# Performance work log

Hardware: AMD Instinct MI355X
Metric: run time of the kernel (lower is better)

Reference implementation:

```python
import jax, jax.numpy as jnp
import numpy as np

DIM = 768
NUM_HEADS = 12
HEAD_DIM = DIM // NUM_HEADS
SCALE = HEAD_DIM ** -0.5


def setup_inputs() -> dict:
    key = jax.random.key(0)
    k_x, k_qw, k_qb, k_pw, k_pb = jax.random.split(key, 5)
    B, S = 4, 2048
    x = jax.random.normal(k_x, (B, S, DIM), dtype=jnp.float32)
    # torch nn.Linear convention: weight shape [out_features, in_features]
    qkv_w = jax.random.normal(k_qw, (2 * DIM, DIM), dtype=jnp.float32) * 0.02
    qkv_b = jax.random.normal(k_qb, (2 * DIM,), dtype=jnp.float32) * 0.02
    proj_w = jax.random.normal(k_pw, (DIM, DIM), dtype=jnp.float32) * 0.02
    proj_b = jax.random.normal(k_pb, (DIM,), dtype=jnp.float32) * 0.02
    return {"x": x, "qkv_w": qkv_w, "qkv_b": qkv_b, "proj_w": proj_w, "proj_b": proj_b}


def reference(x, qkv_w, qkv_b, proj_w, proj_b):
    B, S, D = x.shape
    H, Hd = NUM_HEADS, HEAD_DIM
    # qkv projection -> (B, S, 2*D)
    qkv = jnp.einsum('bsd,ed->bse', x, qkv_w) + qkv_b
    # reshape to (B, S, 2, H, Hd) then split q, v with heads leading: (B, H, S, Hd)
    qkv = qkv.reshape(B, S, 2, H, Hd).transpose(2, 0, 3, 1, 4)
    q, v = qkv[0], qkv[1]
    q = q * SCALE
    # shared Q=K scores: (B, H, S, S)
    attn = jnp.einsum('bhid,bhjd->bhij', q, q)
    attn = jax.nn.softmax(attn, axis=-1)  # attn_drop p=0 (identity)
    out = jnp.einsum('bhij,bhjd->bhid', attn, v)
    out = out.transpose(0, 2, 1, 3).reshape(B, S, D)
    out = jnp.einsum('bsd,ed->bse', out, proj_w) + proj_b  # proj_drop p=0
    return out
```

## Files before the change

### kernel.cpp

```cpp
#include <hip/hip_runtime.h>
#include <hip/hip_bf16.h>

#define NH 12
#define HD 64
#define SEQ 2048
#define DM 768

typedef __attribute__((ext_vector_type(8))) short bf16x8;
typedef __attribute__((ext_vector_type(4))) short bf16x4;
typedef __attribute__((ext_vector_type(4))) float f32x4;

static __device__ __forceinline__ unsigned short f2bf(float f) {
  unsigned int u = __float_as_uint(f);
  u += 0x7fff + ((u >> 16) & 1);
  return (unsigned short)(u >> 16);
}

static __device__ __forceinline__ unsigned cvt_pk_bf16(float lo, float hi) {
  unsigned r;
  asm("v_cvt_pk_bf16_f32 %0, %1, %2" : "=v"(r) : "v"(lo), "v"(hi));
  return r;
}

static __device__ __forceinline__ void gload_lds16(const void* g, void* l) {
  __builtin_amdgcn_global_load_lds(
      (const __attribute__((address_space(1))) void*)g,
      (__attribute__((address_space(3))) void*)l, 16, 0, 0);
}

#define QSCALE 0.15014030f

__global__ __launch_bounds__(256) void cvt3_kernel(
    const float* __restrict__ s0, unsigned short* __restrict__ d0, int n0,
    const float* __restrict__ s1, unsigned short* __restrict__ d1, int n1,
    const float* __restrict__ s2, unsigned short* __restrict__ d2, int n2) {
  int i = blockIdx.x * 256 + threadIdx.x;
  const int stride = gridDim.x * 256;
  const int ntot = n0 + n1 + n2;
  for (; i < ntot; i += stride) {
    const float* src;
    unsigned short* dst;
    int j = i;
    if (j < n0) { src = s0; dst = d0; }
    else if (j < n0 + n1) { j -= n0; src = s1; dst = d1; }
    else { j -= n0 + n1; src = s2; dst = d2; }
    const float4 a = reinterpret_cast<const float4*>(src)[j * 2];
    const float4 b = reinterpret_cast<const float4*>(src)[j * 2 + 1];
    ushort4 lo = make_ushort4(f2bf(a.x), f2bf(a.y), f2bf(a.z), f2bf(a.w));
    ushort4 hi = make_ushort4(f2bf(b.x), f2bf(b.y), f2bf(b.z), f2bf(b.w));
    reinterpret_cast<ushort4*>(dst)[j * 2] = lo;
    reinterpret_cast<ushort4*>(dst)[j * 2 + 1] = hi;
  }
}

__global__ __launch_bounds__(256) void qkv_kernel(
    const unsigned short* __restrict__ xb, const unsigned short* __restrict__ wb,
    const float* __restrict__ bias,
    unsigned short* __restrict__ qb, unsigned short* __restrict__ vtb) {
  __shared__ alignas(16) char As[2][16384];
  __shared__ alignas(16) char Bs[2][16384];
  const int tid = threadIdx.x;
  const int lane = tid & 63, wid = tid >> 6;
  const int wr = wid >> 1, wc = wid & 1;
  const int g = lane >> 4, c = lane & 15;

  const int wg = blockIdx.x;
  const int xcd = wg & 7;
  const int idx = wg >> 3;
  const int m0 = (xcd * 8 + (idx & 7)) * 128;
  const int n0 = (idx >> 3) * 128;
  const char* Ab = (const char*)xb;
  const char* Bb = (const char*)wb;

  auto stage = [&](int kt, int buf) {
    const int k0b = kt * 128;
#pragma unroll
    for (int i = 0; i < 4; ++i) {
      const int o = tid * 16 + i * 4096;
      const int row = o >> 7;
      const int colb = (o & 127) ^ ((row & 7) << 4);
      gload_lds16(Ab + (size_t)(m0 + row) * 1536 + k0b + colb, &As[buf][o]);
      gload_lds16(Bb + (size_t)(n0 + row) * 1536 + k0b + colb, &Bs[buf][o]);
    }
  };

  f32x4 acc[4][4] = {};
  stage(0, 0);

  for (int kt = 0; kt < 12; ++kt) {
    __syncthreads();
    if (kt < 11) stage(kt + 1, (kt + 1) & 1);
    const char* Ap = As[kt & 1];
    const char* Bp = Bs[kt & 1];
    bf16x8 a_f[4][2], b_f[4][2];
#pragma unroll
    for (int i = 0; i < 4; ++i) {
      const int ra = wr * 64 + i * 16 + c;
      const int rb = wc * 64 + i * 16 + c;
      const int sa = (ra & 7) << 4, sb = (rb & 7) << 4;
#pragma unroll
      for (int ks = 0; ks < 2; ++ks) {
        a_f[i][ks] = *reinterpret_cast<const bf16x8*>(Ap + ra * 128 + ((ks * 64 + g * 16) ^ sa));
        b_f[i][ks] = *reinterpret_cast<const bf16x8*>(Bp + rb * 128 + ((ks * 64 + g * 16) ^ sb));
      }
    }
#pragma unroll
    for (int ai = 0; ai < 4; ++ai)
#pragma unroll
      for (int ni = 0; ni < 4; ++ni) {
        acc[ai][ni] = __builtin_amdgcn_mfma_f32_16x16x32_bf16(a_f[ai][0], b_f[ni][0], acc[ai][ni], 0, 0, 0);
        acc[ai][ni] = __builtin_amdgcn_mfma_f32_16x16x32_bf16(a_f[ai][1], b_f[ni][1], acc[ai][ni], 0, 0, 0);
      }
  }

#pragma unroll
  for (int ni = 0; ni < 4; ++ni) {
    const int n = n0 + wc * 64 + ni * 16 + c;
    const float bn = bias[n];
    if (n < DM) {
      const int h = n >> 6, d = n & 63;
#pragma unroll
      for (int ai = 0; ai < 4; ++ai)
#pragma unroll
        for (int r = 0; r < 4; ++r) {
          const int m = m0 + wr * 64 + ai * 16 + g * 4 + r;
          const int bb = m >> 11, s = m & 2047;
          qb[(((size_t)(bb * NH + h)) * SEQ + s) * HD + d] = f2bf((acc[ai][ni][r] + bn) * QSCALE);
        }
    } else {
      const int nn = n - DM;
      const int h = nn >> 6, d = nn & 63;
#pragma unroll
      for (int ai = 0; ai < 4; ++ai) {
        const int m_base = m0 + wr * 64 + ai * 16 + g * 4;
        const int bb = m_base >> 11, s0 = m_base & 2047;
        const int blk = s0 >> 5, off = s0 & 31;
        const int offp = (((off >> 4) & 1) << 2) + (((off >> 2) & 3) << 3);
        ushort4 pk = make_ushort4(f2bf(acc[ai][ni][0] + bn), f2bf(acc[ai][ni][1] + bn),
                                  f2bf(acc[ai][ni][2] + bn), f2bf(acc[ai][ni][3] + bn));
        *reinterpret_cast<ushort4*>(
            &vtb[((size_t)(bb * NH + h) * HD + d) * SEQ + blk * 32 + offp]) = pk;
      }
    }
  }
}

__global__ __launch_bounds__(256, 4) void attn_kernel(
    const unsigned short* __restrict__ qb, const unsigned short* __restrict__ vtb,
    unsigned short* __restrict__ ao) {
  __shared__ alignas(16) char pool[2][16384];

  const int tid = threadIdx.x;
  const int lane = tid & 63, wid = tid >> 6;
  const int g = lane >> 4, c = lane & 15;
  const int wq = wid >> 1, wk = wid & 1;

  const int wg = blockIdx.x;
  const int xcd = wg & 7;
  const int idx = wg >> 3;
  const int bh = xcd * 6 + (idx >> 5);
  const int qs0 = (idx & 31) * 64;
  const size_t base = (size_t)bh * SEQ * HD;

  bf16x8 qf[2][2];
#pragma unroll
  for (int jq = 0; jq < 2; ++jq) {
    const unsigned short* qrow = &qb[base + (size_t)(qs0 + wq * 32 + jq * 16 + c) * HD + g * 8];
    qf[jq][0] = *reinterpret_cast<const bf16x8*>(qrow);
    qf[jq][1] = *reinterpret_cast<const bf16x8*>(qrow + 32);
  }

  const char* qbB = (const char*)qb;
  const char* vtB = (const char*)vtb;
  const int oK0 = tid * 16, oK1 = tid * 16 + 4096;
  const int swK0 = oK0 ^ (((oK0 >> 7) & 7) << 4);
  const int swK1 = oK1 ^ (((oK1 >> 7) & 7) << 4);
  const int rV0 = oK0 >> 7, rV1 = oK1 >> 7;
  const int swV0 = (oK0 & 127) ^ ((rV0 & 7) << 4);
  const int swV1 = (oK1 & 127) ^ ((rV1 & 7) << 4);

  auto stage = [&](int t, int buf) {
    char* P = pool[buf];
    const size_t kQ = base * 2 + (size_t)t * 8192;
    gload_lds16(qbB + kQ + swK0, P + oK0);
    gload_lds16(qbB + kQ + swK1, P + oK1);
    gload_lds16(vtB + ((size_t)(bh * HD + rV0) * SEQ + t * 64) * 2 + swV0, P + 8192 + oK0);
    gload_lds16(vtB + ((size_t)(bh * HD + rV1) * SEQ + t * 64) * 2 + swV1, P + 8192 + oK1);
  };

  float l_p[2] = {0.f, 0.f};
  f32x4 o_acc[4][2] = {};

  const int cswz = (c & 7) << 4;

  stage(0, 0);
  asm volatile("s_waitcnt vmcnt(0)" ::: "memory");
  __builtin_amdgcn_sched_barrier(0);
  __builtin_amdgcn_s_barrier();

  for (int t = 0; t < 32; ++t) {
    const char* P = pool[t & 1];
    if (t < 31) stage(t + 1, (t + 1) & 1);

    f32x4 sa[2][2] = {};
    __builtin_amdgcn_s_setprio(1);
#pragma unroll
    for (int jp = 0; jp < 2; ++jp) {
      const int krow = wk * 32 + jp * 16 + c;
      const bf16x8 kf0 = *reinterpret_cast<const bf16x8*>(P + krow * 128 + ((g * 16) ^ cswz));
      const bf16x8 kf1 = *reinterpret_cast<const bf16x8*>(P + krow * 128 + ((64 + g * 16) ^ cswz));
#pragma unroll
      for (int jq = 0; jq < 2; ++jq) {
        sa[jp][jq] = __builtin_amdgcn_mfma_f32_16x16x32_bf16(kf0, qf[jq][0], sa[jp][jq], 0, 0, 0);
        sa[jp][jq] = __builtin_amdgcn_mfma_f32_16x16x32_bf16(kf1, qf[jq][1], sa[jp][jq], 0, 0, 0);
      }
    }
    __builtin_amdgcn_s_setprio(0);

    bf16x8 pvv[2];
#pragma unroll
    for (int jq = 0; jq < 2; ++jq) {
      float a0 = __builtin_amdgcn_exp2f(sa[0][jq][0]);
      float a1 = __builtin_amdgcn_exp2f(sa[0][jq][1]);
      float a2 = __builtin_amdgcn_exp2f(sa[0][jq][2]);
      float a3 = __builtin_amdgcn_exp2f(sa[0][jq][3]);
      float b0 = __builtin_amdgcn_exp2f(sa[1][jq][0]);
      float b1 = __builtin_amdgcn_exp2f(sa[1][jq][1]);
      float b2 = __builtin_amdgcn_exp2f(sa[1][jq][2]);
      float b3 = __builtin_amdgcn_exp2f(sa[1][jq][3]);
      l_p[jq] += ((a0 + a1) + (a2 + a3)) + ((b0 + b1) + (b2 + b3));
      uint4 u = make_uint4(cvt_pk_bf16(a0, a1), cvt_pk_bf16(a2, a3),
                           cvt_pk_bf16(b0, b1), cvt_pk_bf16(b2, b3));
      pvv[jq] = *reinterpret_cast<bf16x8*>(&u);
    }

    __builtin_amdgcn_s_setprio(1);
#pragma unroll
    for (int dn = 0; dn < 4; ++dn) {
      const int vrow = dn * 16 + c;
      const bf16x8 av = *reinterpret_cast<const bf16x8*>(
          P + 8192 + vrow * 128 + ((wk * 64 + 16 * g) ^ ((vrow & 7) << 4)));
#pragma unroll
      for (int jq = 0; jq < 2; ++jq)
        o_acc[dn][jq] = __builtin_amdgcn_mfma_f32_16x16x32_bf16(av, pvv[jq], o_acc[dn][jq], 0, 0, 0);
    }
    __builtin_amdgcn_s_setprio(0);

    asm volatile("s_waitcnt vmcnt(0)" ::: "memory");
    __builtin_amdgcn_sched_barrier(0);
    __builtin_amdgcn_s_barrier();
  }

#pragma unroll
  for (int jq = 0; jq < 2; ++jq) {
    float v = l_p[jq];
    v += __shfl_xor(v, 16);
    v += __shfl_xor(v, 32);
    l_p[jq] = v;
  }

  float* ex = (float*)(pool[0] + wq * 16384);
  float* exl = ex + 32 * 68;
  if (wk == 1) {
#pragma unroll
    for (int dn = 0; dn < 4; ++dn)
#pragma unroll
      for (int jq = 0; jq < 2; ++jq)
        *reinterpret_cast<f32x4*>(&ex[(jq * 16 + c) * 68 + dn * 16 + 4 * g]) = o_acc[dn][jq];
    if (g == 0) {
      exl[c] = l_p[0];
      exl[16 + c] = l_p[1];
    }
  }
  __syncthreads();
  if (wk == 0) {
    const int b = bh / NH, h = bh % NH;
    float linv[2];
#pragma unroll
    for (int jq = 0; jq < 2; ++jq)
      linv[jq] = __builtin_amdgcn_rcpf(l_p[jq] + exl[jq * 16 + c]);
#pragma unroll
    for (int dn = 0; dn < 4; ++dn)
#pragma unroll
      for (int jq = 0; jq < 2; ++jq) {
        f32x4 o = o_acc[dn][jq];
        o += *reinterpret_cast<const f32x4*>(&ex[(jq * 16 + c) * 68 + dn * 16 + 4 * g]);
        uint2 wv = make_uint2(cvt_pk_bf16(o[0] * linv[jq], o[1] * linv[jq]),
                              cvt_pk_bf16(o[2] * linv[jq], o[3] * linv[jq]));
        *reinterpret_cast<uint2*>(
            &ao[((size_t)b * SEQ + qs0 + wq * 32 + jq * 16 + c) * DM + h * HD + dn * 16 + 4 * g]) = wv;
      }
  }
}

__global__ __launch_bounds__(256) void proj_kernel(
    const unsigned short* __restrict__ ao, const unsigned short* __restrict__ pwb,
    const float* __restrict__ bias, float* __restrict__ out) {
  __shared__ alignas(16) char As[2][8192];
  __shared__ alignas(16) char Bs[2][16384];
  const int tid = threadIdx.x;
  const int lane = tid & 63, wid = tid >> 6;
  const int g = lane >> 4, c = lane & 15;

  const int wg = blockIdx.x;
  const int xcd = wg & 7;
  const int idx = wg >> 3;
  const int m0 = (xcd * 16 + (idx & 15)) * 64;
  const int n0 = (idx >> 4) * 128;
  const char* Ab = (const char*)ao;
  const char* Bb = (const char*)pwb;

  auto stage = [&](int kt, int buf) {
    const int k0b = kt * 128;
#pragma unroll
    for (int i = 0; i < 2; ++i) {
      const int o = tid * 16 + i * 4096;
      const int row = o >> 7;
      const int colb = (o & 127) ^ ((row & 7) << 4);
      gload_lds16(Ab + (size_t)(m0 + row) * 1536 + k0b + colb, &As[buf][o]);
    }
#pragma unroll
    for (int i = 0; i < 4; ++i) {
      const int o = tid * 16 + i * 4096;
      const int row = o >> 7;
      const int colb = (o & 127) ^ ((row & 7) << 4);
      gload_lds16(Bb + (size_t)(n0 + row) * 1536 + k0b + colb, &Bs[buf][o]);
    }
  };

  f32x4 acc[4][2] = {};
  stage(0, 0);

  for (int kt = 0; kt < 12; ++kt) {
    __syncthreads();
    if (kt < 11) stage(kt + 1, (kt + 1) & 1);
    const char* Ap = As[kt & 1];
    const char* Bp = Bs[kt & 1];
    bf16x8 a_f[4][2], b_f[2][2];
#pragma unroll
    for (int i = 0; i < 4; ++i) {
      const int ra = i * 16 + c;
      const int sa = (ra & 7) << 4;
#pragma unroll
      for (int ks = 0; ks < 2; ++ks)
        a_f[i][ks] = *reinterpret_cast<const bf16x8*>(Ap + ra * 128 + ((ks * 64 + g * 16) ^ sa));
    }
#pragma unroll
    for (int j = 0; j < 2; ++j) {
      const int rb = wid * 32 + j * 16 + c;
      const int sb = (rb & 7) << 4;
#pragma unroll
      for (int ks = 0; ks < 2; ++ks)
        b_f[j][ks] = *reinterpret_cast<const bf16x8*>(Bp + rb * 128 + ((ks * 64 + g * 16) ^ sb));
    }
#pragma unroll
    for (int i = 0; i < 4; ++i)
#pragma unroll
      for (int j = 0; j < 2; ++j) {
        acc[i][j] = __builtin_amdgcn_mfma_f32_16x16x32_bf16(a_f[i][0], b_f[j][0], acc[i][j], 0, 0, 0);
        acc[i][j] = __builtin_amdgcn_mfma_f32_16x16x32_bf16(a_f[i][1], b_f[j][1], acc[i][j], 0, 0, 0);
      }
  }

#pragma unroll
  for (int j = 0; j < 2; ++j) {
    const int n = n0 + wid * 32 + j * 16 + c;
    const float bn = bias[n];
#pragma unroll
    for (int i = 0; i < 4; ++i)
#pragma unroll
      for (int r = 0; r < 4; ++r) {
        const int m = m0 + i * 16 + g * 4 + r;
        out[(size_t)m * DM + n] = acc[i][j][r] + bn;
      }
  }
}

extern "C" void kernel_launch(void* const* d_in, const int* in_sizes, int n_in,
                              void* d_out, int out_size, void* d_ws, size_t ws_size,
                              hipStream_t stream) {
  const float* x = (const float*)d_in[0];
  const float* qkv_w = (const float*)d_in[1];
  const float* qkv_b = (const float*)d_in[2];
  const float* proj_w = (const float*)d_in[3];
  const float* proj_b = (const float*)d_in[4];
  float* out = (float*)d_out;

  const size_t elems = (size_t)4 * NH * SEQ * HD;
  unsigned short* qbuf = (unsigned short*)d_ws;
  unsigned short* vtbuf = qbuf + elems;
  unsigned short* xbf = vtbuf + elems;
  unsigned short* aobuf = xbf;
  unsigned short* wqkvbf = xbf + elems;
  unsigned short* wprojbf = wqkvbf + (size_t)2 * DM * DM;

  cvt3_kernel<<<dim3(2048), 256, 0, stream>>>(
      x, xbf, (int)(elems / 8),
      qkv_w, wqkvbf, 2 * DM * DM / 8,
      proj_w, wprojbf, DM * DM / 8);

  qkv_kernel<<<dim3(768), 256, 0, stream>>>(xbf, wqkvbf, qkv_b, qbuf, vtbuf);
  attn_kernel<<<dim3(1536), 256, 0, stream>>>(qbuf, vtbuf, aobuf);
  proj_kernel<<<dim3(768), 256, 0, stream>>>(aobuf, wprojbf, proj_b, out);
}
```

Before: 116.4 us.

## Software-pipeline attention loop: overlap next-tile QK with current softmax·V

Restructures the attention inner loop so the QK^T MFMAs for tile t+1 are issued before the exp/PV work for tile t, using ping-pong score registers. K gets a double buffer and V a triple buffer in LDS, with prefetch issued two tiles ahead after the V fragments are read. The goal is to hide exp latency and global-load latency behind MFMA work. In exchange the kernel uses more LDS (40 KB vs 32 KB) and more registers, which may lower occupancy under launch_bounds(256,4), and it adds an extra syncthreads before the epilogue.

```diff
diff --git a/kernel.cpp b/kernel.cpp
--- a/kernel.cpp
+++ b/kernel.cpp
@@ -148,7 +148,9 @@
 __global__ __launch_bounds__(256, 4) void attn_kernel(
     const unsigned short* __restrict__ qb, const unsigned short* __restrict__ vtb,
     unsigned short* __restrict__ ao) {
-  __shared__ alignas(16) char pool[2][16384];
+  __shared__ alignas(16) char pool[40960];
+  char* Kbuf = pool;
+  char* Vbuf = pool + 16384;
 
   const int tid = threadIdx.x;
   const int lane = tid & 63, wid = tid >> 6;
@@ -179,76 +181,97 @@
   const int swV0 = (oK0 & 127) ^ ((rV0 & 7) << 4);
   const int swV1 = (oK1 & 127) ^ ((rV1 & 7) << 4);
 
-  auto stage = [&](int t, int buf) {
-    char* P = pool[buf];
+  auto stage = [&](int t) {
+    char* Kd = Kbuf + (t & 1) * 8192;
+    char* Vd = Vbuf + (t % 3) * 8192;
     const size_t kQ = base * 2 + (size_t)t * 8192;
-    gload_lds16(qbB + kQ + swK0, P + oK0);
-    gload_lds16(qbB + kQ + swK1, P + oK1);
-    gload_lds16(vtB + ((size_t)(bh * HD + rV0) * SEQ + t * 64) * 2 + swV0, P + 8192 + oK0);
-    gload_lds16(vtB + ((size_t)(bh * HD + rV1) * SEQ + t * 64) * 2 + swV1, P + 8192 + oK1);
+    gload_lds16(qbB + kQ + swK0, Kd + oK0);
+    gload_lds16(qbB + kQ + swK1, Kd + oK1);
+    gload_lds16(vtB + ((size_t)(bh * HD + rV0) * SEQ + t * 64) * 2 + swV0, Vd + oK0);
+    gload_lds16(vtB + ((size_t)(bh * HD + rV1) * SEQ + t * 64) * 2 + swV1, Vd + oK1);
   };
 
   float l_p[2] = {0.f, 0.f};
   f32x4 o_acc[4][2] = {};
-
   const int cswz = (c & 7) << 4;
 
-  stage(0, 0);
-  asm volatile("s_waitcnt vmcnt(0)" ::: "memory");
-  __builtin_amdgcn_sched_barrier(0);
-  __builtin_amdgcn_s_barrier();
-
-  for (int t = 0; t < 32; ++t) {
-    const char* P = pool[t & 1];
-    if (t < 31) stage(t + 1, (t + 1) & 1);
-
-    f32x4 sa[2][2] = {};
+  auto qk = [&](int t1, f32x4 (&s)[2][2]) {
+    const char* Kp = Kbuf + (t1 & 1) * 8192;
+#pragma unroll
+    for (int jp = 0; jp < 2; ++jp)
+#pragma unroll
+      for (int jq = 0; jq < 2; ++jq) s[jp][jq] = f32x4{0.f, 0.f, 0.f, 0.f};
     __builtin_amdgcn_s_setprio(1);
 #pragma unroll
     for (int jp = 0; jp < 2; ++jp) {
       const int krow = wk * 32 + jp * 16 + c;
-      const bf16x8 kf0 = *reinterpret_cast<const bf16x8*>(P + krow * 128 + ((g * 16) ^ cswz));
-      const bf16x8 kf1 = *reinterpret_cast<const bf16x8*>(P + krow * 128 + ((64 + g * 16) ^ cswz));
+      const bf16x8 kf0 = *reinterpret_cast<const bf16x8*>(Kp + krow * 128 + ((g * 16) ^ cswz));
+      const bf16x8 kf1 = *reinterpret_cast<const bf16x8*>(Kp + krow * 128 + ((64 + g * 16) ^ cswz));
 #pragma unroll
       for (int jq = 0; jq < 2; ++jq) {
-        sa[jp][jq] = __builtin_amdgcn_mfma_f32_16x16x32_bf16(kf0, qf[jq][0], sa[jp][jq], 0, 0, 0);
-        sa[jp][jq] = __builtin_amdgcn_mfma_f32_16x16x32_bf16(kf1, qf[jq][1], sa[jp][jq], 0, 0, 0);
+        s[jp][jq] = __builtin_amdgcn_mfma_f32_16x16x32_bf16(kf0, qf[jq][0], s[jp][jq], 0, 0, 0);
+        s[jp][jq] = __builtin_amdgcn_mfma_f32_16x16x32_bf16(kf1, qf[jq][1], s[jp][jq], 0, 0, 0);
       }
     }
     __builtin_amdgcn_s_setprio(0);
-
+  };
+
+  auto smpv = [&](int t, f32x4 (&cur)[2][2]) {
     bf16x8 pvv[2];
 #pragma unroll
     for (int jq = 0; jq < 2; ++jq) {
-      float a0 = __builtin_amdgcn_exp2f(sa[0][jq][0]);
-      float a1 = __builtin_amdgcn_exp2f(sa[0][jq][1]);
-      float a2 = __builtin_amdgcn_exp2f(sa[0][jq][2]);
-      float a3 = __builtin_amdgcn_exp2f(sa[0][jq][3]);
-      float b0 = __builtin_amdgcn_exp2f(sa[1][jq][0]);
-      float b1 = __builtin_amdgcn_exp2f(sa[1][jq][1]);
-      float b2 = __builtin_amdgcn_exp2f(sa[1][jq][2]);
-      float b3 = __builtin_amdgcn_exp2f(sa[1][jq][3]);
+      float a0 = __builtin_amdgcn_exp2f(cur[0][jq][0]);
+      float a1 = __builtin_amdgcn_exp2f(cur[0][jq][1]);
+      float a2 = __builtin_amdgcn_exp2f(cur[0][jq][2]);
+      float a3 = __builtin_amdgcn_exp2f(cur[0][jq][3]);
+      float b0 = __builtin_amdgcn_exp2f(cur[1][jq][0]);
+      float b1 = __builtin_amdgcn_exp2f(cur[1][jq][1]);
+      float b2 = __builtin_amdgcn_exp2f(cur[1][jq][2]);
+      float b3 = __builtin_amdgcn_exp2f(cur[1][jq][3]);
       l_p[jq] += ((a0 + a1) + (a2 + a3)) + ((b0 + b1) + (b2 + b3));
       uint4 u = make_uint4(cvt_pk_bf16(a0, a1), cvt_pk_bf16(a2, a3),
                            cvt_pk_bf16(b0, b1), cvt_pk_bf16(b2, b3));
       pvv[jq] = *reinterpret_cast<bf16x8*>(&u);
     }
-
-    __builtin_amdgcn_s_setprio(1);
+    const char* Vp = Vbuf + (t % 3) * 8192;
+    bf16x8 av[4];
 #pragma unroll
     for (int dn = 0; dn < 4; ++dn) {
       const int vrow = dn * 16 + c;
-      const bf16x8 av = *reinterpret_cast<const bf16x8*>(
-          P + 8192 + vrow * 128 + ((wk * 64 + 16 * g) ^ ((vrow & 7) << 4)));
+      av[dn] = *reinterpret_cast<const bf16x8*>(
+          Vp + vrow * 128 + ((wk * 64 + 16 * g) ^ ((vrow & 7) << 4)));
+    }
+    asm volatile("s_waitcnt lgkmcnt(0)" ::: "memory");
+    __builtin_amdgcn_sched_barrier(0);
+    if (t <= 29) stage(t + 2);
+    __builtin_amdgcn_s_setprio(1);
+#pragma unroll
+    for (int dn = 0; dn < 4; ++dn)
 #pragma unroll
       for (int jq = 0; jq < 2; ++jq)
-        o_acc[dn][jq] = __builtin_amdgcn_mfma_f32_16x16x32_bf16(av, pvv[jq], o_acc[dn][jq], 0, 0, 0);
-    }
+        o_acc[dn][jq] = __builtin_amdgcn_mfma_f32_16x16x32_bf16(av[dn], pvv[jq], o_acc[dn][jq], 0, 0, 0);
     __builtin_amdgcn_s_setprio(0);
-
+  };
+
+  auto iter = [&](int t, f32x4 (&cur)[2][2], f32x4 (&nxt)[2][2]) {
     asm volatile("s_waitcnt vmcnt(0)" ::: "memory");
     __builtin_amdgcn_sched_barrier(0);
     __builtin_amdgcn_s_barrier();
+    if (t < 31) qk(t + 1, nxt);
+    smpv(t, cur);
+  };
+
+  stage(0);
+  stage(1);
+  asm volatile("s_waitcnt vmcnt(4)" ::: "memory");
+  __builtin_amdgcn_sched_barrier(0);
+  __builtin_amdgcn_s_barrier();
+  f32x4 saA[2][2], saB[2][2];
+  qk(0, saA);
+
+  for (int tp = 0; tp < 32; tp += 2) {
+    iter(tp, saA, saB);
+    iter(tp + 1, saB, saA);
   }
 
 #pragma unroll
@@ -258,8 +281,9 @@
     v += __shfl_xor(v, 32);
     l_p[jq] = v;
   }
-
-  float* ex = (float*)(pool[0] + wq * 16384);
+  __syncthreads();
+
+  float* ex = (float*)(pool + wq * 16384);
   float* exl = ex + 32 * 68;
   if (wk == 1) {
 #pragma unroll
```

Measured after the change: 199.4 us. +71.4%, slower.
